# Optimization experiments

Hardware: AMD Instinct MI355X
Metric: run time of the kernel (lower is better)

The kernel has to match this reference:

```python
import jax, jax.numpy as jnp
import numpy as np


def setup_inputs() -> dict:
    key = jax.random.key(0)
    k1, = jax.random.split(key, 1)
    x = jax.random.normal(k1, (32, 64, 64, 256), dtype=jnp.float32)
    gamma = jnp.zeros((1,), dtype=jnp.float32)
    return {"x": x, "gamma": gamma}


def reference(x, gamma):
    # x: [B, H, W, C]
    B, H, W, C = x.shape
    vec_a = x.reshape(B, H * W, C)                 # [B, N, C], N = H*W
    # aTa = vec_a^T @ vec_a -> [B, C, C]
    aTa = jnp.einsum('bnc,bnd->bcd', vec_a, vec_a)
    attn = jax.nn.softmax(aTa, axis=-1)            # softmax over last channel axis
    # aaTa = vec_a @ attn -> [B, N, C]
    aaTa = jnp.einsum('bnc,bcd->bnd', vec_a, attn)
    out = gamma * aaTa.reshape(B, H, W, C) + x
    return out
```

## Files before the change

### kernel.cpp

```cpp
#include <hip/hip_runtime.h>
#include <hip/hip_bf16.h>
#include <stdint.h>


typedef __attribute__((ext_vector_type(8))) short bf16x8s;
typedef __attribute__((ext_vector_type(8))) unsigned short u16x8;
typedef __attribute__((ext_vector_type(4))) unsigned short u16x4;
typedef __attribute__((ext_vector_type(4))) float f32x4;
typedef __attribute__((ext_vector_type(4))) float fl4;
typedef __attribute__((ext_vector_type(4))) uint32_t u32x4;

__device__ __forceinline__ unsigned short f2bf(float f) {
  union { float f; uint32_t u; } v; v.f = f;
  uint32_t r = v.u + 0x7FFFu + ((v.u >> 16) & 1u);
  return (unsigned short)(r >> 16);
}

__device__ __forceinline__ float bf2f(unsigned short h) {
  union { float f; uint32_t u; } v; v.u = ((uint32_t)h) << 16; return v.f;
}

__device__ __forceinline__ uint32_t cvtpk(float lo, float hi) {
  __hip_bfloat162 h = __float22bfloat162_rn(float2{lo, hi});
  union { __hip_bfloat162 h; uint32_t u; } v; v.h = h; return v.u;
}

__device__ __forceinline__ void gload16(const void* g, void* l) {
  __builtin_amdgcn_global_load_lds(
      (const __attribute__((address_space(1))) uint32_t*)g,
      (__attribute__((address_space(3))) uint32_t*)l, 16, 0, 0);
}

__global__ __launch_bounds__(512, 2) void k1_ata(
    const float* __restrict__ x, unsigned short* __restrict__ part) {
  __shared__ __align__(16) unsigned short S[2][256 * 64];

  int bid = blockIdx.x;
  int b = bid >> 3, ks = bid & 7;
  const float* xb = x + ((size_t)b << 20);
  const int nsl = ks * 512;

  int t = threadIdx.x, w = t >> 6, l = t & 63;
  int wm = w >> 1, wn = w & 1;
  int fr = l & 15, fh = l >> 4;

  f32x4 acc[4][8];
#pragma unroll
  for (int m = 0; m < 4; ++m)
#pragma unroll
    for (int n = 0; n < 8; ++n) acc[m][n] = (f32x4)(0.0f);

  fl4 v[8];
  auto LOAD = [&](int kt) {
    const float* s0 = xb + (size_t)(nsl + kt * 64 + w * 8) * 256 + 4 * l;
#pragma unroll
    for (int j = 0; j < 8; ++j) v[j] = *(const fl4*)&s0[(size_t)j * 256];
  };
  auto WRITE = [&](int bsel) {
#pragma unroll
    for (int i = 0; i < 4; ++i) {
      int c = 4 * l + i;
      uint32_t w0 = cvtpk(v[0][i], v[1][i]);
      uint32_t w1 = cvtpk(v[2][i], v[3][i]);
      uint32_t w2 = cvtpk(v[4][i], v[5][i]);
      uint32_t w3 = cvtpk(v[6][i], v[7][i]);
      int byt = c * 128 + ((w * 16) ^ ((c & 7) << 4));
      *(u32x4*)&S[bsel][byt >> 1] = u32x4{w0, w1, w2, w3};
    }
  };

  LOAD(0);
  WRITE(0);
  __syncthreads();

#pragma unroll 1
  for (int kt = 0; kt < 8; ++kt) {
    if (kt < 7) LOAD(kt + 1);
    const unsigned short* Sb = S[kt & 1];
#pragma unroll
    for (int h = 0; h < 2; ++h) {
      bf16x8s afr[4], bfr[8];
#pragma unroll
      for (int m = 0; m < 4; ++m) {
        int row = wm * 64 + m * 16 + fr;
        int byt = row * 128 + ((h * 64 + fh * 16) ^ ((row & 7) << 4));
        afr[m] = *(const bf16x8s*)&Sb[byt >> 1];
      }
#pragma unroll
      for (int n = 0; n < 8; ++n) {
        int row = wn * 128 + n * 16 + fr;
        int byt = row * 128 + ((h * 64 + fh * 16) ^ ((row & 7) << 4));
        bfr[n] = *(const bf16x8s*)&Sb[byt >> 1];
      }
#pragma unroll
      for (int m = 0; m < 4; ++m)
#pragma unroll
        for (int n = 0; n < 8; ++n)
          acc[m][n] = __builtin_amdgcn_mfma_f32_16x16x32_bf16(
              afr[m], bfr[n], acc[m][n], 0, 0, 0);
    }
    if (kt < 7) WRITE((kt + 1) & 1);
    __syncthreads();
  }

  unsigned short* pb = part + ((size_t)bid << 16);
#pragma unroll
  for (int m = 0; m < 4; ++m) {
    int row = wm * 64 + m * 16 + fh * 4;
#pragma unroll
    for (int n = 0; n < 8; ++n) {
      int col = wn * 128 + n * 16 + fr;
#pragma unroll
      for (int i = 0; i < 4; ++i)
        pb[(size_t)(row + i) * 256 + col] = f2bf(acc[m][n][i]);
    }
  }
}

__global__ __launch_bounds__(256) void k2_softmax(
    const unsigned short* __restrict__ part, unsigned short* __restrict__ attnT) {
  __shared__ unsigned short T[256][66];
  int d = blockIdx.x;
  int b    = (d & 7) + 8 * ((d >> 3) >> 2);
  int cblk = (d >> 3) & 3;
  int t = threadIdx.x, w = t >> 6, l = t & 63;
  const unsigned short* pb =
      part + ((size_t)(b * 8) << 16) + (size_t)(cblk * 64) * 256 + 4 * l;

  for (int it = 0; it < 16; ++it) {
    int c = w * 16 + it;
    float s[4] = {0.f, 0.f, 0.f, 0.f};
#pragma unroll
    for (int k = 0; k < 8; ++k) {
      u16x4 vv = *(const u16x4*)&pb[((size_t)k << 16) + (size_t)c * 256];
#pragma unroll
      for (int i = 0; i < 4; ++i) s[i] += bf2f(vv[i]);
    }
    float mx = fmaxf(fmaxf(s[0], s[1]), fmaxf(s[2], s[3]));
    for (int off = 32; off; off >>= 1) mx = fmaxf(mx, __shfl_xor(mx, off));
    float sum = 0.0f;
#pragma unroll
    for (int i = 0; i < 4; ++i) { s[i] = __expf(s[i] - mx); sum += s[i]; }
    for (int off = 32; off; off >>= 1) sum += __shfl_xor(sum, off);
    float inv = 1.0f / sum;
#pragma unroll
    for (int i = 0; i < 4; ++i) T[4 * l + i][c] = f2bf(s[i] * inv);
  }
  __syncthreads();

  unsigned short* ab = attnT + ((size_t)b << 16) + (size_t)t * 256 + cblk * 64;
#pragma unroll
  for (int c8 = 0; c8 < 8; ++c8) {
    u16x8 vv;
#pragma unroll
    for (int j = 0; j < 8; ++j) vv[j] = T[t][c8 * 8 + j];
    *(u16x8*)&ab[c8 * 8] = vv;
  }
}

__global__ __launch_bounds__(256, 4) void k3_av(
    const float* __restrict__ x, const unsigned short* __restrict__ attnT,
    const float* __restrict__ gamma, float* __restrict__ out) {
  __shared__ __align__(16) unsigned short A_s[2][128 * 32];
  __shared__ __align__(16) unsigned short B_s[2][128 * 32];

  int dd = blockIdx.x;
  int xcd = dd & 7, slot = dd >> 3;
  int b = xcd + 8 * (slot >> 6);
  int inner = slot & 63;
  int mt = inner >> 1, dt = inner & 1;
  int n0 = mt << 7, d0 = dt << 7;
  const float* xb = x + ((size_t)b << 20);
  const unsigned short* ab = attnT + ((size_t)b << 16);
  float* ob = out + ((size_t)b << 20);

  int t = threadIdx.x, w = t >> 6, l = t & 63;
  int wm = w >> 1, wn = w & 1;
  int fr = l & 15, fh = l >> 4;

  int ar = t >> 1, ah = t & 1;
  const float* aSrc = xb + (size_t)(n0 + ar) * 256 + ah * 16;
  int brow = l >> 2;
  int bhi = (l & 3) ^ (brow & 3);

  f32x4 acc[4][4];
#pragma unroll
  for (int m = 0; m < 4; ++m)
#pragma unroll
    for (int n = 0; n < 4; ++n) acc[m][n] = (f32x4)(0.0f);

  auto STAGE_A = [&](int bsel, int k0) {
    uint32_t pk[8];
#pragma unroll
    for (int q = 0; q < 4; ++q) {
      fl4 vv = *(const fl4*)&aSrc[k0 + q * 4];
      pk[2 * q]     = cvtpk(vv.x, vv.y);
      pk[2 * q + 1] = cvtpk(vv.z, vv.w);
    }
#pragma unroll
    for (int j = 0; j < 2; ++j) {
      int hi = ah * 2 + j;
      int byt = ar * 64 + ((hi ^ (ar & 3)) << 4);
      *(u32x4*)&A_s[bsel][byt >> 1] =
          u32x4{pk[4 * j], pk[4 * j + 1], pk[4 * j + 2], pk[4 * j + 3]};
    }
  };

  auto STAGE_B = [&](int bsel, int k0) {
#pragma unroll
    for (int r = 0; r < 2; ++r) {
      int seg = r * 4 + w;
      int row = d0 + seg * 16 + brow;
      gload16(&ab[(size_t)row * 256 + k0 + bhi * 8], &B_s[bsel][seg * 512]);
    }
  };

  STAGE_A(0, 0);
  STAGE_B(0, 0);
  __syncthreads();

  int buf = 0;
#pragma unroll 1
  for (int kt = 0; kt < 8; ++kt) {
    if (kt < 7) { STAGE_A(buf ^ 1, (kt + 1) * 32); STAGE_B(buf ^ 1, (kt + 1) * 32); }
    bf16x8s af[4];
#pragma unroll
    for (int m = 0; m < 4; ++m) {
      int row = wm * 64 + m * 16 + fr;
      int byt = row * 64 + ((fh ^ (row & 3)) << 4);
      af[m] = *(const bf16x8s*)&A_s[buf][byt >> 1];
    }
    bf16x8s bfv[4];
#pragma unroll
    for (int n = 0; n < 4; ++n) {
      int dn = wn * 64 + n * 16 + fr;
      int byt = dn * 64 + ((fh ^ (dn & 3)) << 4);
      bfv[n] = *(const bf16x8s*)&B_s[buf][byt >> 1];
    }
#pragma unroll
    for (int m = 0; m < 4; ++m)
#pragma unroll
      for (int n = 0; n < 4; ++n)
        acc[m][n] = __builtin_amdgcn_mfma_f32_16x16x32_bf16(
            af[m], bfv[n], acc[m][n], 0, 0, 0);
    __syncthreads();
    buf ^= 1;
  }

  float g = gamma[0];
#pragma unroll
  for (int m = 0; m < 4; ++m) {
    int row = wm * 64 + m * 16 + fh * 4;
#pragma unroll
    for (int n = 0; n < 4; ++n) {
      int col = d0 + wn * 64 + n * 16 + fr;
#pragma unroll
      for (int i = 0; i < 4; ++i) {
        size_t idx = (size_t)(n0 + row + i) * 256 + col;
        __builtin_nontemporal_store(g * acc[m][n][i] + xb[idx], &ob[idx]);
      }
    }
  }
}

extern "C" void kernel_launch(void* const* d_in, const int* in_sizes, int n_in,
                              void* d_out, int out_size, void* d_ws, size_t ws_size,
                              hipStream_t stream) {
  const float* x     = (const float*)d_in[0];
  const float* gamma = (const float*)d_in[1];
  float* out = (float*)d_out;

  unsigned short* part  = (unsigned short*)((char*)d_out + (size_t)64 * 1024 * 1024);
  unsigned short* attnT = (unsigned short*)d_ws;

  k1_ata<<<256, 512, 0, stream>>>(x, part);
  k2_softmax<<<128, 256, 0, stream>>>(part, attnT);
  k3_av<<<2048, 256, 0, stream>>>(x, attnT, gamma, out);
}
```

Baseline: 110.8 us.

## Fuse softmax into AᵀA kernel via last-block election and widen to 1024 threads

Removes the separate softmax kernel. Each batch's eight split-K blocks increment an atomic counter, and the last one to arrive sums the partial bf16 products, runs the row softmax with four threads per row, and writes the transposed attention matrix through LDS. The AᵀA kernel also moves to 16 waves of 64x64 tiles with a larger LDS buffer, and a memset of the counters is added before launch. This saves a launch and a pass over the partials, but the softmax now runs on only 32 blocks as a tail, and the 64-float per-thread arrays add register pressure.

```diff
diff --git a/kernel.cpp b/kernel.cpp
--- a/kernel.cpp
+++ b/kernel.cpp
@@ -9,6 +9,7 @@
 typedef __attribute__((ext_vector_type(4))) float f32x4;
 typedef __attribute__((ext_vector_type(4))) float fl4;
 typedef __attribute__((ext_vector_type(4))) uint32_t u32x4;
+typedef __attribute__((ext_vector_type(2))) uint32_t u32x2;
 
 __device__ __forceinline__ unsigned short f2bf(float f) {
   union { float f; uint32_t u; } v; v.f = f;
@@ -31,9 +32,11 @@
       (__attribute__((address_space(3))) uint32_t*)l, 16, 0, 0);
 }
 
-__global__ __launch_bounds__(512, 2) void k1_ata(
-    const float* __restrict__ x, unsigned short* __restrict__ part) {
-  __shared__ __align__(16) unsigned short S[2][256 * 64];
+__global__ __launch_bounds__(1024, 4) void k1_ata(
+    const float* __restrict__ x, unsigned short* __restrict__ part,
+    int* __restrict__ cnt, unsigned short* __restrict__ attnT) {
+  __shared__ __align__(16) unsigned char LB[135168];
+  unsigned short (*S)[256 * 64] = (unsigned short (*)[256 * 64])LB;
 
   int bid = blockIdx.x;
   int b = bid >> 3, ks = bid & 7;
@@ -41,20 +44,20 @@
   const int nsl = ks * 512;
 
   int t = threadIdx.x, w = t >> 6, l = t & 63;
-  int wm = w >> 1, wn = w & 1;
+  int wm = w >> 2, wn = w & 3;
   int fr = l & 15, fh = l >> 4;
 
-  f32x4 acc[4][8];
+  f32x4 acc[4][4];
 #pragma unroll
   for (int m = 0; m < 4; ++m)
 #pragma unroll
-    for (int n = 0; n < 8; ++n) acc[m][n] = (f32x4)(0.0f);
-
-  fl4 v[8];
+    for (int n = 0; n < 4; ++n) acc[m][n] = (f32x4)(0.0f);
+
+  fl4 v[4];
   auto LOAD = [&](int kt) {
-    const float* s0 = xb + (size_t)(nsl + kt * 64 + w * 8) * 256 + 4 * l;
-#pragma unroll
-    for (int j = 0; j < 8; ++j) v[j] = *(const fl4*)&s0[(size_t)j * 256];
+    const float* s0 = xb + (size_t)(nsl + kt * 64 + w * 4) * 256 + 4 * l;
+#pragma unroll
+    for (int j = 0; j < 4; ++j) v[j] = *(const fl4*)&s0[(size_t)j * 256];
   };
   auto WRITE = [&](int bsel) {
 #pragma unroll
@@ -62,10 +65,8 @@
       int c = 4 * l + i;
       uint32_t w0 = cvtpk(v[0][i], v[1][i]);
       uint32_t w1 = cvtpk(v[2][i], v[3][i]);
-      uint32_t w2 = cvtpk(v[4][i], v[5][i]);
-      uint32_t w3 = cvtpk(v[6][i], v[7][i]);
-      int byt = c * 128 + ((w * 16) ^ ((c & 7) << 4));
-      *(u32x4*)&S[bsel][byt >> 1] = u32x4{w0, w1, w2, w3};
+      int byt = c * 128 + ((w * 8) ^ ((c & 7) << 4));
+      *(u32x2*)&S[bsel][byt >> 1] = u32x2{w0, w1};
     }
   };
 
@@ -79,7 +80,7 @@
     const unsigned short* Sb = S[kt & 1];
 #pragma unroll
     for (int h = 0; h < 2; ++h) {
-      bf16x8s afr[4], bfr[8];
+      bf16x8s afr[4], bfr[4];
 #pragma unroll
       for (int m = 0; m < 4; ++m) {
         int row = wm * 64 + m * 16 + fr;
@@ -87,15 +88,15 @@
         afr[m] = *(const bf16x8s*)&Sb[byt >> 1];
       }
 #pragma unroll
-      for (int n = 0; n < 8; ++n) {
-        int row = wn * 128 + n * 16 + fr;
+      for (int n = 0; n < 4; ++n) {
+        int row = wn * 64 + n * 16 + fr;
         int byt = row * 128 + ((h * 64 + fh * 16) ^ ((row & 7) << 4));
         bfr[n] = *(const bf16x8s*)&Sb[byt >> 1];
       }
 #pragma unroll
       for (int m = 0; m < 4; ++m)
 #pragma unroll
-        for (int n = 0; n < 8; ++n)
+        for (int n = 0; n < 4; ++n)
           acc[m][n] = __builtin_amdgcn_mfma_f32_16x16x32_bf16(
               afr[m], bfr[n], acc[m][n], 0, 0, 0);
     }
@@ -108,53 +109,73 @@
   for (int m = 0; m < 4; ++m) {
     int row = wm * 64 + m * 16 + fh * 4;
 #pragma unroll
-    for (int n = 0; n < 8; ++n) {
-      int col = wn * 128 + n * 16 + fr;
+    for (int n = 0; n < 4; ++n) {
+      int col = wn * 64 + n * 16 + fr;
 #pragma unroll
       for (int i = 0; i < 4; ++i)
         pb[(size_t)(row + i) * 256 + col] = f2bf(acc[m][n][i]);
     }
   }
-}
-
-__global__ __launch_bounds__(256) void k2_softmax(
-    const unsigned short* __restrict__ part, unsigned short* __restrict__ attnT) {
-  __shared__ unsigned short T[256][66];
-  int d = blockIdx.x;
-  int b    = (d & 7) + 8 * ((d >> 3) >> 2);
-  int cblk = (d >> 3) & 3;
-  int t = threadIdx.x, w = t >> 6, l = t & 63;
-  const unsigned short* pb =
-      part + ((size_t)(b * 8) << 16) + (size_t)(cblk * 64) * 256 + 4 * l;
-
-  for (int it = 0; it < 16; ++it) {
-    int c = w * 16 + it;
-    float s[4] = {0.f, 0.f, 0.f, 0.f};
-#pragma unroll
+
+  __shared__ int elect;
+  if (t == 0) {
+    __threadfence();
+    elect = (atomicAdd(&cnt[b], 1) == 7) ? 1 : 0;
+  }
+  __syncthreads();
+  if (!elect) return;
+  __threadfence();
+
+  unsigned short* T2 = (unsigned short*)LB;
+  const unsigned short* pbase = part + ((size_t)(b * 8) << 16);
+  {
+    int c = t >> 2, q = t & 3;
+    float s[64];
+#pragma unroll
+    for (int e = 0; e < 64; ++e) s[e] = 0.0f;
+#pragma unroll 1
     for (int k = 0; k < 8; ++k) {
-      u16x4 vv = *(const u16x4*)&pb[((size_t)k << 16) + (size_t)c * 256];
-#pragma unroll
-      for (int i = 0; i < 4; ++i) s[i] += bf2f(vv[i]);
-    }
-    float mx = fmaxf(fmaxf(s[0], s[1]), fmaxf(s[2], s[3]));
-    for (int off = 32; off; off >>= 1) mx = fmaxf(mx, __shfl_xor(mx, off));
+      const unsigned short* pk =
+          pbase + ((size_t)k << 16) + (size_t)c * 256 + q * 64;
+#pragma unroll
+      for (int e = 0; e < 8; ++e) {
+        u16x8 vv = *(const u16x8*)&pk[8 * e];
+#pragma unroll
+        for (int i2 = 0; i2 < 8; ++i2) s[8 * e + i2] += bf2f(vv[i2]);
+      }
+    }
+    float mx = s[0];
+#pragma unroll
+    for (int e = 1; e < 64; ++e) mx = fmaxf(mx, s[e]);
+    mx = fmaxf(mx, __shfl_xor(mx, 1));
+    mx = fmaxf(mx, __shfl_xor(mx, 2));
     float sum = 0.0f;
 #pragma unroll
-    for (int i = 0; i < 4; ++i) { s[i] = __expf(s[i] - mx); sum += s[i]; }
-    for (int off = 32; off; off >>= 1) sum += __shfl_xor(sum, off);
+    for (int e = 0; e < 64; ++e) { s[e] = __expf(s[e] - mx); sum += s[e]; }
+    sum += __shfl_xor(sum, 1);
+    sum += __shfl_xor(sum, 2);
     float inv = 1.0f / sum;
 #pragma unroll
-    for (int i = 0; i < 4; ++i) T[4 * l + i][c] = f2bf(s[i] * inv);
+    for (int e = 0; e < 8; ++e) {
+      u16x8 o;
+#pragma unroll
+      for (int i2 = 0; i2 < 8; ++i2) o[i2] = f2bf(s[8 * e + i2] * inv);
+      *(u16x8*)&T2[(size_t)c * 264 + q * 64 + 8 * e] = o;
+    }
   }
   __syncthreads();
-
-  unsigned short* ab = attnT + ((size_t)b << 16) + (size_t)t * 256 + cblk * 64;
-#pragma unroll
-  for (int c8 = 0; c8 < 8; ++c8) {
-    u16x8 vv;
-#pragma unroll
-    for (int j = 0; j < 8; ++j) vv[j] = T[t][c8 * 8 + j];
-    *(u16x8*)&ab[c8 * 8] = vv;
+  {
+    int d = t >> 2, q2 = t & 3;
+    unsigned short* ao =
+        attnT + ((size_t)b << 16) + (size_t)d * 256 + q2 * 64;
+#pragma unroll
+    for (int e = 0; e < 8; ++e) {
+      u16x8 o;
+#pragma unroll
+      for (int i2 = 0; i2 < 8; ++i2)
+        o[i2] = T2[(size_t)(q2 * 64 + 8 * e + i2) * 264 + d];
+      *(u16x8*)&ao[8 * e] = o;
+    }
   }
 }
 
@@ -271,9 +292,10 @@
   float* out = (float*)d_out;
 
   unsigned short* part  = (unsigned short*)((char*)d_out + (size_t)64 * 1024 * 1024);
+  int*            cnt   = (int*)((char*)d_out + (size_t)100 * 1024 * 1024);
   unsigned short* attnT = (unsigned short*)d_ws;
 
-  k1_ata<<<256, 512, 0, stream>>>(x, part);
-  k2_softmax<<<128, 256, 0, stream>>>(part, attnT);
+  hipMemsetAsync(cnt, 0, 32 * sizeof(int), stream);
+  k1_ata<<<256, 1024, 0, stream>>>(x, part, cnt, attnT);
   k3_av<<<2048, 256, 0, stream>>>(x, attnT, gamma, out);
 }
```

New measurement: 190.8 us. +72.1%, slower.
